# Kernel optimization log

Measured on AMD Instinct MI355X. Metric: run time of the kernel, lower is better.

The kernel has to match this reference:

```python
import jax, jax.numpy as jnp
import numpy as np

SCORE_THRESHOLD = 0.5
IOU_THRESHOLD = 0.5
N = 8192
IMG = 640.0


def setup_inputs() -> dict:
    key = jax.random.key(0)
    k1, k2, k3 = jax.random.split(key, 3)
    # valid xyxy boxes on a 640px canvas: x2 > x1, y2 > y1
    xy1 = jax.random.uniform(k1, (N, 2), dtype=jnp.float32) * (IMG - 64.0)
    wh = jax.random.uniform(k2, (N, 2), dtype=jnp.float32) * 96.0 + 4.0
    xyxy = jnp.concatenate([xy1, xy1 + wh], axis=1)  # [N,4]
    person_conf = jax.random.uniform(k3, (N,), dtype=jnp.float32)  # [N]
    return {"xyxy": xyxy, "person_conf": person_conf}


def _pairwise_iou(boxes):
    # boxes: [N,4] xyxy -> iou: [N,N]
    x1, y1, x2, y2 = boxes[:, 0], boxes[:, 1], boxes[:, 2], boxes[:, 3]
    area = (x2 - x1) * (y2 - y1)  # [N]
    ix1 = jnp.maximum(x1[:, None], x1[None, :])
    iy1 = jnp.maximum(y1[:, None], y1[None, :])
    ix2 = jnp.minimum(x2[:, None], x2[None, :])
    iy2 = jnp.minimum(y2[:, None], y2[None, :])
    iw = jnp.maximum(ix2 - ix1, 0.0)
    ih = jnp.maximum(iy2 - iy1, 0.0)
    inter = iw * ih
    union = area[:, None] + area[None, :] - inter
    return inter / jnp.maximum(union, 1e-9)


def reference(xyxy, person_conf):
    # score-threshold filter (as a mask to stay jit-compatible / fixed shape)
    valid = person_conf >= SCORE_THRESHOLD  # [N]
    # sort by score descending; invalid boxes sink to the bottom
    sort_scores = jnp.where(valid, person_conf, -jnp.inf)
    order = jnp.argsort(-sort_scores)  # [N]
    boxes_s = xyxy[order]              # [N,4]
    scores_s = person_conf[order]      # [N]
    valid_s = valid[order]             # [N]

    iou = _pairwise_iou(boxes_s)  # [N,N]
    idx = jnp.arange(N)

    def body(i, keep):
        # box i (if still kept) suppresses lower-scored overlapping boxes
        sup = keep[i] & (iou[i] > IOU_THRESHOLD) & (idx > i)
        return keep & ~sup

    keep = jax.lax.fori_loop(0, N, body, valid_s)  # [N] bool

    boxes_and_scores = jnp.concatenate([boxes_s, scores_s[:, None]], axis=1)  # [N,5]
    out = jnp.where(keep[:, None], boxes_and_scores, 0.0)  # suppressed rows zeroed
    return out, keep
```

## Files before the change

### kernel.cpp

```cpp
#include <hip/hip_runtime.h>

typedef unsigned long long u64;
typedef unsigned int u32;

static constexpr int N = 8192;
static constexpr int NW = N / 64;
static constexpr int CAPE = 12288;
static constexpr int EPT = CAPE / 1024;


__device__ __forceinline__ u64 make_key(float s, int i) {
  u32 adj = (s >= 0.5f) ? (__float_as_uint(s) + 1u) : 0u;
  return ((u64)adj << 32) | (u64)(u32)(N - 1 - i);
}

__global__ __launch_bounds__(256)
void rank_kernel(const float* __restrict__ conf, u32* __restrict__ rank_partial) {
  __shared__ u64 sk[1024];
  const int t = threadIdx.x;
  const int jb = blockIdx.y;
  for (int k = t; k < 1024; k += 256) {
    int j = jb * 1024 + k;
    sk[k] = make_key(conf[j], j);
  }
  __syncthreads();
  const int i = blockIdx.x * 256 + t;
  const u64 ki = make_key(conf[i], i);
  int cnt = 0;
  #pragma unroll 8
  for (int k = 0; k < 1024; ++k) cnt += (sk[k] > ki);
  rank_partial[jb * N + i] = (u32)cnt;
}

__global__ __launch_bounds__(256)
void scatter_kernel(const float4* __restrict__ xyxy, const float* __restrict__ conf,
                    const u32* __restrict__ rank_partial,
                    float4* __restrict__ boxes_s, float* __restrict__ scores_s,
                    float* __restrict__ areas_s, int* __restrict__ ecount) {
  #pragma clang fp contract(off)
  const int i = blockIdx.x * 256 + threadIdx.x;
  if (i == 0) *ecount = 0;
  u32 r = 0;
  #pragma unroll
  for (int jb = 0; jb < 8; ++jb) r += rank_partial[jb * N + i];
  float4 b = xyxy[i];
  boxes_s[r] = b;
  scores_s[r] = conf[i];
  areas_s[r] = (b.z - b.x) * (b.w - b.y);
}

__global__ __launch_bounds__(256)
void mask_kernel(const float4* __restrict__ boxes_s, const float* __restrict__ areas_s,
                 const float* __restrict__ scores_s,
                 u64* __restrict__ edgeW, u32* __restrict__ edgeM,
                 int* __restrict__ ecount) {
  #pragma clang fp contract(off)
  __shared__ float4 cb[4][64];
  __shared__ float ca[4][64];
  const int wave = threadIdx.x >> 6;
  const int t = threadIdx.x & 63;
  const int xb = blockIdx.x * 4 + wave;
  const int yb = blockIdx.y;
  if (xb < yb) return;
  if (scores_s[xb * 64] < 0.5f) return;
  cb[wave][t] = boxes_s[xb * 64 + t];
  ca[wave][t] = areas_s[xb * 64 + t];
  const int i = yb * 64 + t;
  const float4 rb = boxes_s[i];
  const float ra = areas_s[i];
  const float sc_i = scores_s[i];
  const int jbase = xb * 64;
  u64 w = 0;
  for (int q = 0; q < 64; ++q) {
    float4 c = cb[wave][q];
    float ix1 = fmaxf(rb.x, c.x);
    float iy1 = fmaxf(rb.y, c.y);
    float ix2 = fminf(rb.z, c.z);
    float iy2 = fminf(rb.w, c.w);
    float iw = fmaxf(ix2 - ix1, 0.0f);
    float ih = fmaxf(iy2 - iy1, 0.0f);
    float inter = iw * ih;
    float uni = fmaxf((ra + ca[wave][q]) - inter, 1e-9f);
    float iou = inter / uni;
    if ((iou > 0.5f) && (jbase + q > i)) w |= (1ull << q);
  }
  if (sc_i < 0.5f) w = 0;
  u64 nz = __ballot(w != 0ull);
  if (!nz) return;
  int base = 0;
  if (t == 0) base = atomicAdd(ecount, __popcll(nz));
  base = __shfl(base, 0);
  if (w) {
    int idx = base + __popcll(nz & ((1ull << t) - 1ull));
    if (idx < CAPE) {
      edgeW[idx] = w;
      edgeM[idx] = (u32)i | ((u32)xb << 16);
    }
  }
}

__global__ __launch_bounds__(1024)
void reduce_write_kernel(const u64* __restrict__ edgeW, const u32* __restrict__ edgeM,
                         const int* __restrict__ ecount,
                         const float* __restrict__ scores_s,
                         const float4* __restrict__ boxes_s,
                         float* __restrict__ out) {
  __shared__ u32 removed32[2 * NW];
  __shared__ u32 keep32[2 * NW];
  __shared__ u64 validm[NW];
  __shared__ int chg[2];
  const int tid = threadIdx.x;
  const int lane = tid & 63;

  if (tid == 0) { chg[0] = 0; chg[1] = 0; }
  for (int p = tid; p < N; p += 1024) {
    u64 b = __ballot(scores_s[p] >= 0.5f);
    if (lane == 0) validm[p >> 6] = b;
  }
  int E = *ecount;
  if (E > CAPE) E = CAPE;

  u64 ew[EPT]; u32 em[EPT]; int ne = 0;
  #pragma unroll
  for (int k = 0; k < EPT; ++k) {
    int e = tid + k * 1024;
    if (e < E) { ew[k] = edgeW[e]; em[k] = edgeM[e]; ne = k + 1; }
    else       { ew[k] = 0; em[k] = 0; }
  }
  __syncthreads();
  if (tid < 256) keep32[tid] = ((const u32*)validm)[tid];
  __syncthreads();

  for (int it = 0; it < N; ++it) {
    if (tid < 256) removed32[tid] = 0;
    if (tid == 0) chg[(it + 1) & 1] = 0;
    __syncthreads();
    #pragma unroll
    for (int k = 0; k < EPT; ++k) {
      if (k < ne) {
        int row = em[k] & 0xffff;
        if ((keep32[row >> 5] >> (row & 31)) & 1u) {
          int x = em[k] >> 16;
          atomicOr(&removed32[2 * x],     (u32)ew[k]);
          atomicOr(&removed32[2 * x + 1], (u32)(ew[k] >> 32));
        }
      }
    }
    __syncthreads();
    if (tid < 256) {
      u32 nk = ((const u32*)validm)[tid] & ~removed32[tid];
      if (nk != keep32[tid]) { keep32[tid] = nk; chg[it & 1] = 1; }
    }
    __syncthreads();
    if (!chg[it & 1]) break;
  }

  for (int s = tid; s < N; s += 1024) {
    bool keep = (keep32[s >> 5] >> (s & 31)) & 1u;
    float4 b = boxes_s[s];
    float sc = scores_s[s];
    float* row = out + (u64)s * 5;
    if (keep) {
      row[0] = b.x; row[1] = b.y; row[2] = b.z; row[3] = b.w; row[4] = sc;
      out[N * 5 + s] = 1.0f;
    } else {
      row[0] = 0.0f; row[1] = 0.0f; row[2] = 0.0f; row[3] = 0.0f; row[4] = 0.0f;
      out[N * 5 + s] = 0.0f;
    }
  }
}

extern "C" void kernel_launch(void* const* d_in, const int* in_sizes, int n_in,
                              void* d_out, int out_size, void* d_ws, size_t ws_size,
                              hipStream_t stream) {
  const float4* xyxy = (const float4*)d_in[0];
  const float* conf  = (const float*)d_in[1];
  char* ws = (char*)d_ws;
  float4* boxes_s   = (float4*)(ws + 0);
  float*  scores_s  = (float*)(ws + 131072);
  float*  areas_s   = (float*)(ws + 163840);
  int*    ecount    = (int*)(ws + 196608);
  u64*    edgeW     = (u64*)(ws + 196672);
  u32*    edgeM     = (u32*)(ws + 294976);
  u32*    rank_partial = (u32*)(ws + 344128);
  float*  out       = (float*)d_out;

  dim3 rg(N / 256, 8);
  rank_kernel<<<rg, 256, 0, stream>>>(conf, rank_partial);
  scatter_kernel<<<N / 256, 256, 0, stream>>>(xyxy, conf, rank_partial,
                                              boxes_s, scores_s, areas_s, ecount);
  dim3 mg(NW / 4, NW);
  mask_kernel<<<mg, 256, 0, stream>>>(boxes_s, areas_s, scores_s,
                                      edgeW, edgeM, ecount);
  reduce_write_kernel<<<1, 1024, 0, stream>>>(edgeW, edgeM, ecount,
                                              scores_s, boxes_s, out);
}
```

Measured before the change: 115.4 us.

## Replace fixed-point NMS iteration with ordered word-by-word sweep

The single-block reduce kernel used to iterate to a fixed point, applying all edges each round until the keep set stopped changing. It now sweeps the 64-box words in score order: one thread resolves the suppressions inside each diagonal word serially using a shared 64x64 bit matrix, then all threads apply the off-diagonal edges whose source row lies in that word. This replaces a data-dependent number of full passes with a single ordered pass over only the valid words. The rank kernel is also split into 32 smaller segments to give more parallel blocks. The sweep block shrinks to 256 threads, so each thread holds 48 edges in registers and the serial per-word loop adds latency.

```diff
diff --git a/kernel.cpp b/kernel.cpp
--- a/kernel.cpp
+++ b/kernel.cpp
@@ -6,7 +6,10 @@
 static constexpr int N = 8192;
 static constexpr int NW = N / 64;
 static constexpr int CAPE = 12288;
-static constexpr int EPT = CAPE / 1024;
+static constexpr int RSEG = 32;
+static constexpr int RT = 256;
+static constexpr int EPT = CAPE / RT;
+static constexpr int DCAP = 96;
 
 
 __device__ __forceinline__ u64 make_key(float s, int i) {
@@ -16,19 +19,17 @@
 
 __global__ __launch_bounds__(256)
 void rank_kernel(const float* __restrict__ conf, u32* __restrict__ rank_partial) {
-  __shared__ u64 sk[1024];
+  __shared__ u64 sk[256];
   const int t = threadIdx.x;
   const int jb = blockIdx.y;
-  for (int k = t; k < 1024; k += 256) {
-    int j = jb * 1024 + k;
-    sk[k] = make_key(conf[j], j);
-  }
+  const int j = jb * 256 + t;
+  sk[t] = make_key(conf[j], j);
   __syncthreads();
   const int i = blockIdx.x * 256 + t;
   const u64 ki = make_key(conf[i], i);
   int cnt = 0;
   #pragma unroll 8
-  for (int k = 0; k < 1024; ++k) cnt += (sk[k] > ki);
+  for (int k = 0; k < 256; ++k) cnt += (sk[k] > ki);
   rank_partial[jb * N + i] = (u32)cnt;
 }
 
@@ -42,7 +43,7 @@
   if (i == 0) *ecount = 0;
   u32 r = 0;
   #pragma unroll
-  for (int jb = 0; jb < 8; ++jb) r += rank_partial[jb * N + i];
+  for (int jb = 0; jb < RSEG; ++jb) r += rank_partial[jb * N + i];
   float4 b = xyxy[i];
   boxes_s[r] = b;
   scores_s[r] = conf[i];
@@ -99,64 +100,98 @@
   }
 }
 
-__global__ __launch_bounds__(1024)
-void reduce_write_kernel(const u64* __restrict__ edgeW, const u32* __restrict__ edgeM,
-                         const int* __restrict__ ecount,
-                         const float* __restrict__ scores_s,
-                         const float4* __restrict__ boxes_s,
-                         float* __restrict__ out) {
-  __shared__ u32 removed32[2 * NW];
-  __shared__ u32 keep32[2 * NW];
+__global__ __launch_bounds__(256)
+void sweep_write_kernel(const u64* __restrict__ edgeW, const u32* __restrict__ edgeM,
+                        const int* __restrict__ ecount,
+                        const float* __restrict__ scores_s,
+                        const float4* __restrict__ boxes_s,
+                        float* __restrict__ out) {
   __shared__ u64 validm[NW];
-  __shared__ int chg[2];
+  __shared__ u64 keepm[NW];
+  __shared__ u32 rem32[2 * NW];
+  __shared__ u64 intraM[DCAP];
+  __shared__ u64 D[DCAP][64];
+  __shared__ int NvS;
   const int tid = threadIdx.x;
   const int lane = tid & 63;
 
-  if (tid == 0) { chg[0] = 0; chg[1] = 0; }
-  for (int p = tid; p < N; p += 1024) {
+  if (tid == 0) NvS = 0;
+  if (tid < NW) keepm[tid] = 0;
+  rem32[tid] = 0;
+  if (tid < DCAP) intraM[tid] = 0;
+  __syncthreads();
+
+  for (int p = tid; p < N; p += RT) {
     u64 b = __ballot(scores_s[p] >= 0.5f);
-    if (lane == 0) validm[p >> 6] = b;
-  }
+    if (lane == 0) {
+      validm[p >> 6] = b;
+      atomicAdd(&NvS, __popcll(b));
+    }
+  }
+
   int E = *ecount;
   if (E > CAPE) E = CAPE;
 
-  u64 ew[EPT]; u32 em[EPT]; int ne = 0;
+  u64 ew[EPT]; u32 em[EPT];
   #pragma unroll
   for (int k = 0; k < EPT; ++k) {
-    int e = tid + k * 1024;
-    if (e < E) { ew[k] = edgeW[e]; em[k] = edgeM[e]; ne = k + 1; }
-    else       { ew[k] = 0; em[k] = 0; }
-  }
-  __syncthreads();
-  if (tid < 256) keep32[tid] = ((const u32*)validm)[tid];
-  __syncthreads();
-
-  for (int it = 0; it < N; ++it) {
-    if (tid < 256) removed32[tid] = 0;
-    if (tid == 0) chg[(it + 1) & 1] = 0;
+    int e = tid + k * RT;
+    if (e < E) { ew[k] = edgeW[e]; em[k] = edgeM[e]; }
+    else       { ew[k] = 0; em[k] = 0xFFFFFFFFu; }
+  }
+  __syncthreads();
+
+  #pragma unroll
+  for (int k = 0; k < EPT; ++k) {
+    u32 m_ = em[k];
+    int row = (int)(m_ & 0xffffu);
+    int x   = (int)(m_ >> 16);
+    int rw  = row >> 6;
+    if (x == rw && rw < DCAP) {
+      D[rw][row & 63] = ew[k];
+      atomicOr(&intraM[rw], 1ull << (row & 63));
+      em[k] = 0xFFFFFFFFu;
+    }
+  }
+  __syncthreads();
+
+  int NWv = (NvS + 63) >> 6;
+  if (NWv > DCAP) NWv = DCAP;
+
+  for (int y = 0; y < NWv; ++y) {
     __syncthreads();
+    if (tid == 0) {
+      u64 rm = ((u64)rem32[2 * y + 1] << 32) | (u64)rem32[2 * y];
+      u64 kk = validm[y] & ~rm;
+      u64 m = intraM[y] & kk;
+      while (m) {
+        int q = __ffsll((long long)m) - 1;
+        kk &= ~D[y][q];
+        m &= ~(1ull << q);
+        m &= kk;
+      }
+      keepm[y] = kk;
+    }
+    __syncthreads();
+    const u64 kpy = keepm[y];
     #pragma unroll
     for (int k = 0; k < EPT; ++k) {
-      if (k < ne) {
-        int row = em[k] & 0xffff;
-        if ((keep32[row >> 5] >> (row & 31)) & 1u) {
-          int x = em[k] >> 16;
-          atomicOr(&removed32[2 * x],     (u32)ew[k]);
-          atomicOr(&removed32[2 * x + 1], (u32)(ew[k] >> 32));
+      if (k * RT < E) {
+        u32 m_ = em[k];
+        if (((m_ >> 6) & 0x3FFu) == (u32)y) {
+          if ((kpy >> (m_ & 63u)) & 1ull) {
+            u32 x = m_ >> 16;
+            atomicOr(&rem32[2 * x],     (u32)ew[k]);
+            atomicOr(&rem32[2 * x + 1], (u32)(ew[k] >> 32));
+          }
         }
       }
     }
-    __syncthreads();
-    if (tid < 256) {
-      u32 nk = ((const u32*)validm)[tid] & ~removed32[tid];
-      if (nk != keep32[tid]) { keep32[tid] = nk; chg[it & 1] = 1; }
-    }
-    __syncthreads();
-    if (!chg[it & 1]) break;
-  }
-
-  for (int s = tid; s < N; s += 1024) {
-    bool keep = (keep32[s >> 5] >> (s & 31)) & 1u;
+  }
+  __syncthreads();
+
+  for (int s = tid; s < N; s += RT) {
+    bool keep = (keepm[s >> 6] >> (s & 63)) & 1ull;
     float4 b = boxes_s[s];
     float sc = scores_s[s];
     float* row = out + (u64)s * 5;
@@ -185,13 +220,13 @@
   u32*    rank_partial = (u32*)(ws + 344128);
   float*  out       = (float*)d_out;
 
-  dim3 rg(N / 256, 8);
+  dim3 rg(N / 256, RSEG);
   rank_kernel<<<rg, 256, 0, stream>>>(conf, rank_partial);
   scatter_kernel<<<N / 256, 256, 0, stream>>>(xyxy, conf, rank_partial,
                                               boxes_s, scores_s, areas_s, ecount);
   dim3 mg(NW / 4, NW);
   mask_kernel<<<mg, 256, 0, stream>>>(boxes_s, areas_s, scores_s,
                                       edgeW, edgeM, ecount);
-  reduce_write_kernel<<<1, 1024, 0, stream>>>(edgeW, edgeM, ecount,
-                                              scores_s, boxes_s, out);
-}
+  sweep_write_kernel<<<1, 256, 0, stream>>>(edgeW, edgeM, ecount,
+                                            scores_s, boxes_s, out);
+}
```

Measured after the change: 231.1 us. 2x slower.
